# Performance work log

Hardware: AMD Instinct MI355X
Metric: run time of the kernel (lower is better)

The kernel has to match this reference:

```python
import jax, jax.numpy as jnp
import numpy as np

B, T, D, H, V = 512, 40, 300, 200, 50257  # batch, max_length, embed_size, lstm_dimension, vocab
FORGET_BIAS = 1.0  # TF1 LSTMCell default


def setup_inputs() -> dict:
    key = jax.random.key(0)
    ks = jax.random.split(key, 8)
    s = 0.02
    return {
        "input_ids": jax.random.randint(ks[0], (B, T), 0, V, dtype=jnp.int32),
        "lengths": jax.random.randint(ks[1], (B,), 1, T + 1, dtype=jnp.int32),
        "emb": (jax.random.normal(ks[2], (V, D)) * s).astype(jnp.float32),
        "Wx": (jax.random.normal(ks[3], (D, 4 * H)) * s).astype(jnp.float32),
        "Wh": (jax.random.normal(ks[4], (H, 4 * H)) * s).astype(jnp.float32),
        "b": jnp.zeros((4 * H,), jnp.float32),
        "U": (jax.random.normal(ks[5], (H, D)) * s).astype(jnp.float32),
        "b1": jnp.zeros((D,), jnp.float32),
        "b2": jnp.zeros((V,), jnp.float32),
    }


def lstm_last_cell(x, lengths, Wx, Wh, b):
    """TF1 LSTMCell (gate order i, j, f, o; forget_bias=1) unrolled like
    dynamic_rnn with sequence_length: state frozen past each row's length.
    Returns final cell state c of shape [B, H]."""
    Bq = x.shape[0]
    Hq = Wh.shape[0]
    xt = jnp.transpose(x, (1, 0, 2))                      # [T, B, D]
    xproj = xt @ Wx + b                                    # [T, B, 4H] precomputed input GEMM
    tmask = (jnp.arange(x.shape[1])[:, None] < lengths[None, :])[..., None]  # [T, B, 1]

    def step(carry, inp):
        c, h = carry
        xp, m = inp
        gates = xp + h @ Wh                                # [B, 4H]
        i, j, f, o = jnp.split(gates, 4, axis=-1)
        c_new = jax.nn.sigmoid(f + FORGET_BIAS) * c + jax.nn.sigmoid(i) * jnp.tanh(j)
        h_new = jax.nn.sigmoid(o) * jnp.tanh(c_new)
        c = jnp.where(m, c_new, c)
        h = jnp.where(m, h_new, h)
        return (c, h), None

    init = (jnp.zeros((Bq, Hq), x.dtype), jnp.zeros((Bq, Hq), x.dtype))
    (c, _h), _ = jax.lax.scan(step, init, (xproj, tmask))
    return c


def reference(input_ids, lengths, emb, Wx, Wh, b, U, b1, b2):
    x = emb[input_ids]                                     # [B, T, D] embedding lookup
    c = lstm_last_cell(x, lengths, Wx, Wh, b)              # [B, H] final cell state (state.c)
    h1 = jax.nn.relu(c @ U + b1)                           # [B, D]
    # dropout with keep_prob=1 at eval -> identity
    return h1 @ emb.T + b2                                 # [B, V] tied-weight logits
```

## Files before the change

### kernel.cpp

```cpp
#include <hip/hip_runtime.h>
#include <stdint.h>

#define TT_  40
#define GP_  896
#define HKP_ 224
#define V_   50257
#define VP_  50432

typedef __attribute__((ext_vector_type(4))) float f32x4;
typedef __attribute__((ext_vector_type(8))) short s16x8;

__device__ __forceinline__ ushort bfrn(float f) {
  union { float f; uint32_t u; } x; x.f = f;
  return (ushort)((x.u + 0x7fffu + ((x.u >> 16) & 1u)) >> 16);
}
__device__ __forceinline__ float bl16(uint32_t u) { return __uint_as_float(u << 16); }
__device__ __forceinline__ float bh16(uint32_t u) { return __uint_as_float(u & 0xffff0000u); }
__device__ __forceinline__ float sigm(float x) { return 1.f / (1.f + __expf(-x)); }
__device__ __forceinline__ float tanh_f(float x) { return 1.f - 2.f / (__expf(2.f*x) + 1.f); }

template<int N> struct IC { static constexpr int v = N; };

__global__ void k_prep_emb(const float* __restrict__ emb, ushort* __restrict__ emb_bf) {
  const int idx = blockIdx.x * 256 + threadIdx.x;
  const int v = idx / 80, kc = idx % 80;
  ushort4 o = {0, 0, 0, 0};
  if (v < V_ && kc < 75) {
    const float4 f = *(const float4*)(emb + (size_t)v * 300 + kc * 4);
    o.x = bfrn(f.x); o.y = bfrn(f.y); o.z = bfrn(f.z); o.w = bfrn(f.w);
  }
  *(ushort4*)(emb_bf + (size_t)v * 320 + kc * 4) = o;
}

__global__ void k_prep_small(const float* __restrict__ Wx, const float* __restrict__ Wh,
                             const float* __restrict__ U, ushort* __restrict__ Wxp,
                             ushort* __restrict__ Whp, float* __restrict__ Ut) {
  int idx = blockIdx.x * 256 + threadIdx.x;
  if (idx < 896 * 320) {
    const int colp = idx / 320, k = idx % 320;
    const int n = colp >> 2, g = colp & 3;
    const float v = (colp < 800 && k < 300) ? Wx[(size_t)k * 800 + g * 200 + n] : 0.f;
    Wxp[idx] = bfrn(v);
    return;
  }
  idx -= 896 * 320;
  if (idx < 896 * 224) {
    const int colp = idx / 224, k = idx % 224;
    const int n = colp >> 2, g = colp & 3;
    const float v = (colp < 800 && k < 200) ? Wh[(size_t)k * 800 + g * 200 + n] : 0.f;
    Whp[idx] = bfrn(v);
    return;
  }
  idx -= 896 * 224;
  if (idx < 300 * 200) {
    const int d = idx / 200, h = idx % 200;
    Ut[idx] = U[(size_t)h * 300 + d];
  }
}

__global__ __launch_bounds__(256) void k_xproj(
    const int* __restrict__ ids, const ushort* __restrict__ emb_bf,
    const ushort* __restrict__ Wxp, const float* __restrict__ bias,
    ushort* __restrict__ xp) {
  __shared__ ushort bsm[70 * 512];
  const int tid = threadIdx.x;
  const int w = tid >> 6, lane = tid & 63;
  const int l15 = lane & 15, q = lane >> 4;
  const int wgm = blockIdx.x, wgn = blockIdx.y;
  const int t = wgm >> 3;
  const int bbase = (wgm & 7) << 6;
  const int n0 = wgn * 112;

  for (int s = w; s < 70; s += 4) {
    const int tl = s / 10, kb = s % 10;
    const s16x8 v = *(const s16x8*)(Wxp + (size_t)(n0 + tl * 16 + l15) * 320 + kb * 32 + q * 8);
    *(s16x8*)(&bsm[s * 512 + lane * 8]) = v;
  }
  const int brow = bbase + w * 16 + l15;
  const int id = ids[brow * TT_ + t];
  const ushort* arow = emb_bf + (size_t)id * 320;
  __syncthreads();

  f32x4 acc[7];
  const f32x4 z = {0.f, 0.f, 0.f, 0.f};
#pragma unroll
  for (int tl = 0; tl < 7; ++tl) acc[tl] = z;
  for (int kb = 0; kb < 10; ++kb) {
    const s16x8 af = *(const s16x8*)(arow + kb * 32 + q * 8);
#pragma unroll
    for (int tl = 0; tl < 7; ++tl) {
      const s16x8 bfv = *(const s16x8*)(&bsm[(tl * 10 + kb) * 512 + lane * 8]);
      acc[tl] = __builtin_amdgcn_mfma_f32_16x16x32_bf16(af, bfv, acc[tl], 0, 0, 0);
    }
  }
  const int rowbase = t * 512 + bbase + w * 16 + q * 4;
#pragma unroll
  for (int tl = 0; tl < 7; ++tl) {
    const int colp = n0 + tl * 16 + l15;
    const float bv = (colp < 800) ? bias[(colp & 3) * 200 + (colp >> 2)] : 0.f;
#pragma unroll
    for (int r = 0; r < 4; ++r)
      xp[(size_t)(rowbase + r) * GP_ + colp] = bfrn(acc[tl][r] + bv);
  }
}

__global__ __launch_bounds__(512) __attribute__((amdgpu_waves_per_eu(2, 2)))
void k_lstm(
    const ushort* __restrict__ xp, const ushort* __restrict__ Whp,
    const int* __restrict__ lengths, const float* __restrict__ Ut,
    const float* __restrict__ b1v, ushort* __restrict__ h1bf) {
  __shared__ ushort h_lds[2][3584];
  __shared__ ushort wh6_lds[28672];
  __shared__ ushort xp_lds[2][14336];
  __shared__ float  c_lds[16 * 228];

  const int tid = threadIdx.x;
  const int w = tid >> 6, lane = tid & 63;
  const int l15 = lane & 15, q = lane >> 4;
  const int b0 = blockIdx.x << 4;
  const int len = lengths[b0 + l15];

  s16x8 whf[7][6];
#pragma unroll
  for (int tl = 0; tl < 7; ++tl) {
    const ushort* wr = Whp + (size_t)((w * 7 + tl) * 16 + l15) * HKP_;
#pragma unroll
    for (int kb = 0; kb < 6; ++kb)
      whf[tl][kb] = *(const s16x8*)(wr + kb * 32 + q * 8);
    *(s16x8*)(&wh6_lds[(w * 7 + tl) * 512 + lane * 8]) = *(const s16x8*)(wr + 192 + q * 8);
  }
  for (int i = tid; i < 3584; i += 512) ((uint32_t*)h_lds)[i] = 0;
  for (int i = tid; i < 16 * 228; i += 512) c_lds[i] = 0.f;

  int xpoff[7], hwoff[7];
  unsigned nokm = 0;
#pragma unroll
  for (int tl = 0; tl < 7; ++tl) {
    const int T0 = w * 7 + tl;
    const int cch = 112 * l15 + 2 * T0 + (q >> 1);
    xpoff[tl] = ((cch ^ ((cch >> 4) & 7)) << 4) | ((q & 1) << 3);
    const int n = T0 * 4 + q;
    if (n < 200) nokm |= (1u << tl);
    hwoff[tl] = (n >> 5) * 1024 + (l15 + (((n >> 3) & 3) << 4)) * 16 + (n & 7) * 2;
  }
  const int cidx = l15 * 228 + w * 28 + q;

  auto stage = [&](int t, int buf) {
    const char* src = (const char*)(xp + (size_t)(t * 512 + b0) * GP_);
#pragma unroll
    for (int r = 0; r < 4; ++r) {
      const int slot0 = r * 512 + w * 64;
      if (slot0 < 1792) {
        const int p = slot0 + lane;
        const int c = p ^ ((p >> 4) & 7);
        __builtin_amdgcn_global_load_lds(
            (const __attribute__((address_space(1))) uint32_t*)(src + c * 16),
            (__attribute__((address_space(3))) uint32_t*)((char*)(&xp_lds[buf][0]) + slot0 * 16),
            16, 0, 0);
      }
    }
  };

  stage(0, 0);
  __syncthreads();

  auto step = [&](int t, auto BUFC) {
    constexpr int BUF = decltype(BUFC)::v;
    if (t + 1 < TT_) stage(t + 1, BUF ^ 1);
    f32x4 acc[7];
    const f32x4 z = {0.f, 0.f, 0.f, 0.f};
#pragma unroll
    for (int tl = 0; tl < 7; ++tl) acc[tl] = z;
#pragma unroll
    for (int kb = 0; kb < 7; ++kb) {
      const s16x8 hh = *(const s16x8*)(&h_lds[BUF][kb * 512 + lane * 8]);
#pragma unroll
      for (int tl = 0; tl < 7; ++tl) {
        s16x8 a;
        if (kb < 6) a = whf[tl][kb];
        else        a = *(const s16x8*)(&wh6_lds[(w * 7 + tl) * 512 + lane * 8]);
        acc[tl] = __builtin_amdgcn_mfma_f32_16x16x32_bf16(a, hh, acc[tl], 0, 0, 0);
      }
    }
    const bool act = (t < len);
#pragma unroll
    for (int tl = 0; tl < 7; ++tl) {
      const uint2 xv = *(const uint2*)((const char*)(&xp_lds[BUF][0]) + xpoff[tl]);
      const float g0 = acc[tl][0] + bl16(xv.x);
      const float g1 = acc[tl][1] + bh16(xv.x);
      const float g2 = acc[tl][2] + bl16(xv.y);
      const float g3 = acc[tl][3] + bh16(xv.y);
      const bool nok = (nokm >> tl) & 1;
      ushort hv = *(const ushort*)((const char*)(&h_lds[BUF][0]) + hwoff[tl]);
      if (act && nok) {
        const float cold = c_lds[cidx + 4 * tl];
        const float sf = sigm(g2 + 1.f);
        const float si = sigm(g0);
        const float tj = tanh_f(g1);
        const float cn = sf * cold + si * tj;
        c_lds[cidx + 4 * tl] = cn;
        hv = bfrn(sigm(g3) * tanh_f(cn));
      }
      if (nok)
        *(ushort*)((char*)(&h_lds[BUF ^ 1][0]) + hwoff[tl]) = hv;
    }
    __syncthreads();
  };

  for (int tt = 0; tt < TT_ / 2; ++tt) {
    step(2 * tt,     IC<0>{});
    step(2 * tt + 1, IC<1>{});
  }

  for (int i = tid; i < 4800; i += 512) {
    const int col = i >> 4, row = i & 15;
    const float* ut = Ut + col * 200;
    const float* cr = &c_lds[row * 228];
    float s = 0.f;
    for (int k = 0; k < 200; k += 4) {
      const float4 cc = *(const float4*)(cr + k);
      const float4 uu = *(const float4*)(ut + k);
      s += cc.x * uu.x + cc.y * uu.y + cc.z * uu.z + cc.w * uu.w;
    }
    s += b1v[col];
    h1bf[(size_t)(b0 + row) * 320 + col] = bfrn(fmaxf(s, 0.f));
  }
  if (tid < 320) {
    const int row = tid & 15, col = 300 + (tid >> 4);
    h1bf[(size_t)(b0 + row) * 320 + col] = 0;
  }
}

__global__ __launch_bounds__(256) void k_out(
    const ushort* __restrict__ h1bf, const ushort* __restrict__ emb_bf,
    const float* __restrict__ b2, float* __restrict__ out) {
  const int tid = threadIdx.x;
  const int w = tid >> 6, lane = tid & 63;
  const int l15 = lane & 15, q = lane >> 4;
  const int m0 = blockIdx.y << 6;
  const int n0 = blockIdx.x * 256 + w * 64;
  f32x4 acc[4][4];
  const f32x4 z = {0.f, 0.f, 0.f, 0.f};
#pragma unroll
  for (int a = 0; a < 4; ++a)
#pragma unroll
    for (int b = 0; b < 4; ++b) acc[a][b] = z;
  for (int kb = 0; kb < 10; ++kb) {
    s16x8 af[4], bfv[4];
#pragma unroll
    for (int mt = 0; mt < 4; ++mt)
      af[mt] = *(const s16x8*)(h1bf + (size_t)(m0 + mt * 16 + l15) * 320 + kb * 32 + q * 8);
#pragma unroll
    for (int nt = 0; nt < 4; ++nt)
      bfv[nt] = *(const s16x8*)(emb_bf + (size_t)(n0 + nt * 16 + l15) * 320 + kb * 32 + q * 8);
#pragma unroll
    for (int mt = 0; mt < 4; ++mt)
#pragma unroll
      for (int nt = 0; nt < 4; ++nt)
        acc[mt][nt] = __builtin_amdgcn_mfma_f32_16x16x32_bf16(af[mt], bfv[nt], acc[mt][nt], 0, 0, 0);
  }
#pragma unroll
  for (int nt = 0; nt < 4; ++nt) {
    const int col = n0 + nt * 16 + l15;
    if (col < V_) {
      const float bb = b2[col];
#pragma unroll
      for (int mt = 0; mt < 4; ++mt) {
        const int row = m0 + mt * 16 + q * 4;
#pragma unroll
        for (int r = 0; r < 4; ++r)
          out[(size_t)(row + r) * V_ + col] = acc[mt][nt][r] + bb;
      }
    }
  }
}

extern "C" void kernel_launch(void* const* d_in, const int* in_sizes, int n_in,
                              void* d_out, int out_size, void* d_ws, size_t ws_size,
                              hipStream_t stream) {
  (void)in_sizes; (void)n_in; (void)out_size; (void)ws_size;
  const int*   ids  = (const int*)d_in[0];
  const int*   lens = (const int*)d_in[1];
  const float* emb  = (const float*)d_in[2];
  const float* Wx   = (const float*)d_in[3];
  const float* Wh   = (const float*)d_in[4];
  const float* bg   = (const float*)d_in[5];
  const float* U    = (const float*)d_in[6];
  const float* b1   = (const float*)d_in[7];
  const float* b2   = (const float*)d_in[8];
  float* out = (float*)d_out;

  char* ws = (char*)d_ws;
  ushort* emb_bf = (ushort*)(ws);
  ushort* Wxp    = (ushort*)(ws + 32276480);
  ushort* Whp    = (ushort*)(ws + 32849920);
  float*  Ut     = (float*)(ws + 33251328);
  ushort* h1bf   = (ushort*)(ws + 33491328);
  ushort* xp     = (ushort*)((char*)d_out + 66226176);

  k_prep_emb  <<<15760, 256, 0, stream>>>(emb, emb_bf);
  k_prep_small<<<2139,  256, 0, stream>>>(Wx, Wh, U, Wxp, Whp, Ut);
  k_xproj     <<<dim3(320, 8), 256, 0, stream>>>(ids, emb_bf, Wxp, bg, xp);
  k_lstm      <<<32, 512, 0, stream>>>(xp, Whp, lens, Ut, b1, h1bf);
  k_out       <<<dim3(197, 8), 256, 0, stream>>>(h1bf, emb_bf, b2, out);
}
```

Before: 374.9 us.

## Load LSTM input projections directly from global into registers instead of LDS staging

Removes the double-buffered LDS staging of the precomputed input projection, which used async global-to-LDS loads. Each thread now loads its seven 8-byte gate slices straight from global memory at the start of every timestep, before the recurrent MFMA loop. It also swaps the waves-per-EU attribute for an explicit 256-VGPR budget when the compiler supports it. This frees LDS and address math, but the global load latency now sits on the serial recurrence path with no prefetch one step ahead.

```diff
diff --git a/kernel.cpp b/kernel.cpp
--- a/kernel.cpp
+++ b/kernel.cpp
@@ -104,14 +104,23 @@
   }
 }
 
-__global__ __launch_bounds__(512) __attribute__((amdgpu_waves_per_eu(2, 2)))
+#if defined(__has_attribute)
+#if __has_attribute(amdgpu_num_vgpr)
+#define KLSTM_REGS __attribute__((amdgpu_num_vgpr(256)))
+#else
+#define KLSTM_REGS __attribute__((amdgpu_waves_per_eu(2, 2)))
+#endif
+#else
+#define KLSTM_REGS
+#endif
+
+__global__ __launch_bounds__(512) KLSTM_REGS
 void k_lstm(
     const ushort* __restrict__ xp, const ushort* __restrict__ Whp,
     const int* __restrict__ lengths, const float* __restrict__ Ut,
     const float* __restrict__ b1v, ushort* __restrict__ h1bf) {
   __shared__ ushort h_lds[2][3584];
   __shared__ ushort wh6_lds[28672];
-  __shared__ ushort xp_lds[2][14336];
   __shared__ float  c_lds[16 * 228];
 
   const int tid = threadIdx.x;
@@ -132,41 +141,27 @@
   for (int i = tid; i < 3584; i += 512) ((uint32_t*)h_lds)[i] = 0;
   for (int i = tid; i < 16 * 228; i += 512) c_lds[i] = 0.f;
 
-  int xpoff[7], hwoff[7];
+  int hwoff[7];
   unsigned nokm = 0;
 #pragma unroll
   for (int tl = 0; tl < 7; ++tl) {
     const int T0 = w * 7 + tl;
-    const int cch = 112 * l15 + 2 * T0 + (q >> 1);
-    xpoff[tl] = ((cch ^ ((cch >> 4) & 7)) << 4) | ((q & 1) << 3);
     const int n = T0 * 4 + q;
     if (n < 200) nokm |= (1u << tl);
     hwoff[tl] = (n >> 5) * 1024 + (l15 + (((n >> 3) & 3) << 4)) * 16 + (n & 7) * 2;
   }
   const int cidx = l15 * 228 + w * 28 + q;
-
-  auto stage = [&](int t, int buf) {
-    const char* src = (const char*)(xp + (size_t)(t * 512 + b0) * GP_);
-#pragma unroll
-    for (int r = 0; r < 4; ++r) {
-      const int slot0 = r * 512 + w * 64;
-      if (slot0 < 1792) {
-        const int p = slot0 + lane;
-        const int c = p ^ ((p >> 4) & 7);
-        __builtin_amdgcn_global_load_lds(
-            (const __attribute__((address_space(1))) uint32_t*)(src + c * 16),
-            (__attribute__((address_space(3))) uint32_t*)((char*)(&xp_lds[buf][0]) + slot0 * 16),
-            16, 0, 0);
-      }
-    }
-  };
-
-  stage(0, 0);
+  const char* xbase = (const char*)xp + (size_t)(b0 + l15) * (GP_ * 2) + w * 224 + q * 8;
+
   __syncthreads();
 
   auto step = [&](int t, auto BUFC) {
     constexpr int BUF = decltype(BUFC)::v;
-    if (t + 1 < TT_) stage(t + 1, BUF ^ 1);
+    const char* xpp = xbase + (size_t)t * (512 * GP_ * 2);
+    uint2 xv[7];
+#pragma unroll
+    for (int tl = 0; tl < 7; ++tl) xv[tl] = *(const uint2*)(xpp + tl * 32);
+
     f32x4 acc[7];
     const f32x4 z = {0.f, 0.f, 0.f, 0.f};
 #pragma unroll
@@ -185,11 +180,10 @@
     const bool act = (t < len);
 #pragma unroll
     for (int tl = 0; tl < 7; ++tl) {
-      const uint2 xv = *(const uint2*)((const char*)(&xp_lds[BUF][0]) + xpoff[tl]);
-      const float g0 = acc[tl][0] + bl16(xv.x);
-      const float g1 = acc[tl][1] + bh16(xv.x);
-      const float g2 = acc[tl][2] + bl16(xv.y);
-      const float g3 = acc[tl][3] + bh16(xv.y);
+      const float g0 = acc[tl][0] + bl16(xv[tl].x);
+      const float g1 = acc[tl][1] + bh16(xv[tl].x);
+      const float g2 = acc[tl][2] + bl16(xv[tl].y);
+      const float g3 = acc[tl][3] + bh16(xv[tl].y);
       const bool nok = (nokm >> tl) & 1;
       ushort hv = *(const ushort*)((const char*)(&h_lds[BUF][0]) + hwoff[tl]);
       if (act && nok) {
```

Result: slower. 384.9 us (+2.7%).
